# Performance work log

Hardware: AMD Instinct MI355X
Metric: run time of the kernel (lower is better)

## Reference

```python
import jax, jax.numpy as jnp
import numpy as np

B, N_PER, DEG, F_IN, F_HID = 64, 1024, 16, 128, 128
E = B * N_PER * DEG  # 1,048,576 edges, grouped per graph


def setup_inputs() -> dict:
    key = jax.random.key(0)
    ks = jax.random.split(key, 16)
    n_total = B * N_PER
    x = jax.random.normal(ks[0], (n_total, F_IN), dtype=jnp.float32)
    # edges are random within each graph block
    local = jax.random.randint(ks[1], (2, E), 0, N_PER)
    offs = (jnp.arange(E, dtype=jnp.int64) // (N_PER * DEG)) * N_PER
    edge_index = (local.astype(jnp.int64) + offs[None, :])
    edge_weight = jax.random.uniform(ks[2], (E,), dtype=jnp.float32)
    batch_index = jnp.repeat(jnp.arange(B, dtype=jnp.int64), N_PER)
    s = 1.0 / np.sqrt(F_HID)
    params = {
        'W1': jax.random.normal(ks[3], (F_IN, F_HID)) * s,
        'b1': jnp.zeros((F_HID,), jnp.float32),
        'p1': jax.random.normal(ks[4], (F_HID,)) * s,
        'W2': jax.random.normal(ks[5], (F_HID, F_HID)) * s,
        'b2': jnp.zeros((F_HID,), jnp.float32),
        'p2': jax.random.normal(ks[6], (F_HID,)) * s,
        'W3': jax.random.normal(ks[7], (F_HID, F_HID)) * s,
        'b3': jnp.zeros((F_HID,), jnp.float32),
        'p3': jax.random.normal(ks[8], (F_HID,)) * s,
        'Wo': jax.random.normal(ks[9], (2 * F_HID, 1)) * s,
        'bo': jnp.zeros((1,), jnp.float32),
    }
    return {'x': x, 'edge_index': edge_index, 'edge_weight': edge_weight,
            'batch_index': batch_index, **params}


def _gcn_conv(x, src, dst, w, W, b):
    # GCNConv with add_self_loops=True, symmetric normalization, edge_weight.
    n = x.shape[0]
    xW = x @ W
    deg = jnp.zeros((n,), x.dtype).at[dst].add(w) + 1.0  # +1 from self-loop fill
    dinv = jax.lax.rsqrt(deg)
    norm = dinv[src] * w * dinv[dst]
    agg = jnp.zeros_like(xW).at[dst].add(norm[:, None] * xW[src])
    return agg + (dinv * dinv)[:, None] * xW + b  # self-loop term + bias


def _topk_pool(x, src, dst, w, p, n, k):
    # TopKPooling with nonlinearity=sigmoid, equal-size graphs (n -> k nodes).
    f = x.shape[1]
    xr = x.reshape(B, n, f)
    score = jax.nn.sigmoid((xr @ p) / jnp.linalg.norm(p))  # [B, n]
    vals, perm = jax.lax.top_k(score, k)                    # per-graph top-k
    xn = jnp.take_along_axis(xr, perm[:, :, None], axis=1) * vals[:, :, None]
    # inverse map old local idx -> new local idx (-1 if dropped)
    inv = jnp.full((B, n), -1, dtype=jnp.int32)
    inv = inv.at[jnp.arange(B)[:, None], perm].set(jnp.arange(k, dtype=jnp.int32)[None, :])
    g = src // n
    sl = inv[g, src % n]
    dl = inv[dst // n, dst % n]
    keep = (sl >= 0) & (dl >= 0)
    # dropped edges are masked to node 0 with weight 0 (contribute nothing)
    src2 = jnp.where(keep, g * k + sl, 0)
    dst2 = jnp.where(keep, (dst // n) * k + dl, 0)
    w2 = jnp.where(keep, w, jnp.zeros((), w.dtype))
    return xn.reshape(B * k, f), src2, dst2, w2


def reference(x, edge_index, edge_weight, batch_index,
              W1, b1, p1, W2, b2, p2, W3, b3, p3, Wo, bo):
    src, dst = edge_index[0], edge_index[1]
    w = edge_weight
    n = N_PER
    h = _gcn_conv(x, src, dst, w, W1, b1)
    h, src, dst, w = _topk_pool(h, src, dst, w, p1, n, n // 2); n //= 2
    h = jax.nn.relu(h)
    h = _gcn_conv(h, src, dst, w, W2, b2)
    h, src, dst, w = _topk_pool(h, src, dst, w, p2, n, n // 2); n //= 2
    h = jax.nn.relu(h)
    h = _gcn_conv(h, src, dst, w, W3, b3)
    h, src, dst, w = _topk_pool(h, src, dst, w, p3, n, n // 2); n //= 2
    h = jax.nn.relu(h)
    hr = h.reshape(B, n, -1)
    cat = jnp.concatenate([hr.max(axis=1), hr.mean(axis=1)], axis=1)  # gmp || gap
    out = jax.nn.sigmoid(cat @ Wo + bo)
    return out, cat
```

## Files before the change

kernel.cpp:

```cpp
#include <hip/hip_runtime.h>

#define NB 64
#define EDGES 1048576
#define NTOT  65536

struct __align__(8) CsrE { int s; float w; };

using bf16x8 = __attribute__((ext_vector_type(8))) short;
using f32x4  = __attribute__((ext_vector_type(4))) float;

__global__ void k_zerof(float* __restrict__ p, int n){
  int i=blockIdx.x*256+threadIdx.x; if(i<n) p[i]=0.f;
}

__device__ inline void split1(float x, unsigned &hi16, unsigned &lo16){
  unsigned b=__float_as_uint(x);
  unsigned h=(b+0x7FFFu+((b>>16)&1u))&0xFFFF0000u;
  float lf=x-__uint_as_float(h);
  unsigned lb=__float_as_uint(lf);
  hi16=h>>16;
  lo16=(lb+0x7FFFu+((lb>>16)&1u))>>16;
}

__device__ inline void split8(const float4&u, const float4&v, bf16x8&hi, bf16x8&lo){
  float e[8]={u.x,u.y,u.z,u.w,v.x,v.y,v.z,v.w};
  #pragma unroll
  for(int j=0;j<8;++j){
    unsigned h16,l16; split1(e[j],h16,l16);
    hi[j]=(short)h16; lo[j]=(short)l16;
  }
}

__global__ __launch_bounds__(256) void k_wpack(const float* __restrict__ W1,
        const float* __restrict__ W2, const float* __restrict__ W3,
        unsigned* __restrict__ outp){
  int b=blockIdx.x, m=b>>3;
  const float* W = (m==0)?W1:((m==1)?W2:W3);
  unsigned* o = outp + m*16384;
  for(int t=(b&7)*256+threadIdx.x; t<8192; t+=2048){
    int i=t&3, l=(t>>2)&63, c=(t>>8)&7, q=(t>>11)&3;
    int col=c*16+(l&15);
    int k0=q*32+((l>>4)<<3)+i*2;
    float x0=W[k0*128+col], x1=W[(k0+1)*128+col];
    unsigned h0,l0,h1,l1;
    split1(x0,h0,l0); split1(x1,h1,l1);
    int base=((q*8+c)*2)*256;
    o[base + l*4 + i]       = (h1<<16)|h0;
    o[base + 256 + l*4 + i] = (l1<<16)|l0;
  }
}

template<bool G, int S>
__global__ __launch_bounds__(256) void mm_mfma(const float* __restrict__ X,
        const unsigned* __restrict__ Wpk, const int* __restrict__ selold,
        const float* __restrict__ score, float* __restrict__ Y, int gshift){
  __shared__ __align__(16) unsigned Wl[16384];
  const int RPB = 64*S;
  int b=blockIdx.x;
  int row0b;
  if(G){
    int xcd=b&7, slot=b>>3, bpg=1<<gshift;
    int graph=xcd*8+(slot>>gshift), idx=slot&(bpg-1);
    row0b = graph*(bpg*RPB) + idx*RPB;
  } else row0b = b*RPB;
  for(int t=threadIdx.x;t<4096;t+=256)
    ((uint4*)Wl)[t]=((const uint4*)Wpk)[t];
  const int wave=threadIdx.x>>6, lane=threadIdx.x&63;
  const int row0 = row0b + wave*(16*S);
  const int lrow=lane&15, lko=(lane>>4)<<3;
  int orow[S]; float scr[S];
  #pragma unroll
  for(int s=0;s<S;++s){
    int rr=row0+s*16+lrow;
    orow[s]=G?selold[rr]:rr;
    scr[s]=G?score[orow[s]]:1.f;
  }
  const f32x4 vzero={0.f,0.f,0.f,0.f};
  f32x4 acc[S][8];
  #pragma unroll
  for(int s=0;s<S;++s){
    #pragma unroll
    for(int c=0;c<8;++c) acc[s][c]=vzero;
  }
  __syncthreads();
  const char* wb=(const char*)Wl + lane*16;
  float4 u[S],v[S];
  #pragma unroll
  for(int s=0;s<S;++s){
    const float* xp=X+(size_t)orow[s]*128+lko;
    u[s]=*(const float4*)xp; v[s]=*(const float4*)(xp+4);
  }
  #pragma unroll
  for(int q=0;q<4;++q){
    float4 un[S],vn[S];
    if(q<3){
      #pragma unroll
      for(int s=0;s<S;++s){
        const float* xp=X+(size_t)orow[s]*128+(q+1)*32+lko;
        un[s]=*(const float4*)xp; vn[s]=*(const float4*)(xp+4);
      }
    }
    bf16x8 Ah[S],Al[S];
    #pragma unroll
    for(int s=0;s<S;++s){
      if(G){
        u[s].x=fmaxf(u[s].x*scr[s],0.f); u[s].y=fmaxf(u[s].y*scr[s],0.f);
        u[s].z=fmaxf(u[s].z*scr[s],0.f); u[s].w=fmaxf(u[s].w*scr[s],0.f);
        v[s].x=fmaxf(v[s].x*scr[s],0.f); v[s].y=fmaxf(v[s].y*scr[s],0.f);
        v[s].z=fmaxf(v[s].z*scr[s],0.f); v[s].w=fmaxf(v[s].w*scr[s],0.f);
      }
      split8(u[s],v[s],Ah[s],Al[s]);
    }
    #pragma unroll
    for(int c=0;c<8;++c){
      const bf16x8 bh=*(const bf16x8*)(wb + (q*8+c)*2048);
      const bf16x8 bl=*(const bf16x8*)(wb + (q*8+c)*2048 + 1024);
      #pragma unroll
      for(int s=0;s<S;++s){
        acc[s][c]=__builtin_amdgcn_mfma_f32_16x16x32_bf16(Ah[s],bh,acc[s][c],0,0,0);
        acc[s][c]=__builtin_amdgcn_mfma_f32_16x16x32_bf16(Al[s],bh,acc[s][c],0,0,0);
        acc[s][c]=__builtin_amdgcn_mfma_f32_16x16x32_bf16(Ah[s],bl,acc[s][c],0,0,0);
      }
    }
    if(q<3){
      #pragma unroll
      for(int s=0;s<S;++s){ u[s]=un[s]; v[s]=vn[s]; }
    }
  }
  const int dcol=lane&15, dr0=(lane>>4)<<2;
  #pragma unroll
  for(int s=0;s<S;++s){
    #pragma unroll
    for(int c=0;c<8;++c){
      #pragma unroll
      for(int r=0;r<4;++r){
        Y[(size_t)(row0+s*16+dr0+r)*128 + c*16 + dcol]=acc[s][c][r];
      }
    }
  }
}

__global__ __launch_bounds__(1024) void k_count(const int* __restrict__ edst,
        const float* __restrict__ ew, int* __restrict__ chunkcnt, float* __restrict__ chunkw){
  __shared__ int lc[1024];
  __shared__ float lw[1024];
  int b=blockIdx.x, i=threadIdx.x;
  int xcd=b&7, slot=b>>3;
  int graph=xcd*8+(slot&7), chunk=slot>>3;
  int e0=graph*16384+chunk*4096;
  lc[i]=0; lw[i]=0.f;
  __syncthreads();
  for(int e=e0+i; e<e0+4096; e+=1024){
    int dl=edst[e]&1023;
    atomicAdd(&lc[dl],1);
    atomicAdd(&lw[dl],ew[e]);
  }
  __syncthreads();
  chunkcnt[chunk*65536+graph*1024+i]=lc[i];
  chunkw  [chunk*65536+graph*1024+i]=lw[i];
}

__global__ __launch_bounds__(1024) void k_scan_graph(const int* __restrict__ chunkcnt,
        const float* __restrict__ chunkw, int* __restrict__ rowptr,
        float* __restrict__ dinv1, int* __restrict__ chunkfill){
  __shared__ int wsum[16];
  int g=blockIdx.x, i=threadIdx.x;
  int lane=i&63, w=i>>6;
  int o=g*1024+i;
  int c0=chunkcnt[o], c1=chunkcnt[65536+o], c2=chunkcnt[131072+o], c3=chunkcnt[196608+o];
  int c=c0+c1+c2+c3;
  float ws = chunkw[o]+chunkw[65536+o]+chunkw[131072+o]+chunkw[196608+o];
  int v=c;
  #pragma unroll
  for(int off=1;off<64;off<<=1){ int t=__shfl_up(v,off,64); if(lane>=off) v+=t; }
  if(lane==63) wsum[w]=v;
  __syncthreads();
  int base=0;
  for(int k=0;k<w;++k) base+=wsum[k];
  int excl=base+v-c;
  int e0=g*16384;
  int r0=e0+excl;
  rowptr[o]=r0;
  chunkfill[o]       =r0;
  chunkfill[65536+o] =r0+c0;
  chunkfill[131072+o]=r0+c0+c1;
  chunkfill[196608+o]=r0+c0+c1+c2;
  dinv1[o]=rsqrtf(ws+1.0f);
  if(g==63 && i==1023) rowptr[65536]=EDGES;
}

__global__ __launch_bounds__(1024) void k_scatter2(const int* __restrict__ esrc,
        const int* __restrict__ edst, const float* __restrict__ ew,
        const int* __restrict__ chunkfill, CsrE* __restrict__ csr){
  __shared__ int lc[1024];
  int b=blockIdx.x, i=threadIdx.x;
  int xcd=b&7, slot=b>>3;
  int graph=xcd*8+(slot&7), chunk=slot>>3;
  int e0=graph*16384+chunk*4096;
  lc[i]=chunkfill[chunk*65536+graph*1024+i];
  __syncthreads();
  for(int e=e0+i; e<e0+4096; e+=1024){
    int dl=edst[e]&1023;
    int pos=atomicAdd(&lc[dl],1);
    CsrE ce; ce.s=esrc[e]; ce.w=ew[e];
    csr[pos]=ce;
  }
}

template<bool F>
__global__ __launch_bounds__(256) void k_gather(const float* __restrict__ xw, const CsrE* __restrict__ csr,
        const int* __restrict__ rowptr, const int* __restrict__ map, const int* __restrict__ inv,
        const float* __restrict__ dinvv, const float* __restrict__ bias, const float* __restrict__ p,
        float* __restrict__ h, float* __restrict__ score, int gshift, int ns){
  int wv=threadIdx.x>>6, half=(threadIdx.x>>5)&1, hl=threadIdx.x&31;
  int b=blockIdx.x, xcd=b&7, slot=b>>3, bpg=1<<gshift;
  int graph=xcd*8+(slot>>gshift), idx=slot&(bpg-1);
  int v = graph*(bpg<<3) + (idx<<3) + wv*2 + half;
  if(v>=ns) return;
  int d0 = F? map[v] : v;
  float dv=dinvv[v];
  int rs=rowptr[d0], re=rowptr[d0+1];
  const int f4=hl*4;
  float4 accA={0.f,0.f,0.f,0.f}, accB={0.f,0.f,0.f,0.f};
  for(int base=rs; base<re; base+=32){
    int len=re-base; if(len>32) len=32;
    int sidx=0; float cf=0.f;
    if(hl<len){
      CsrE en=csr[base+hl];
      int s=en.s; bool live=true;
      if(F){ int t=inv[s]; live=(t>=0); s=live?t:0; }
      if(live){ sidx=s; cf=dinvv[s]*en.w; }
    }
    int len4=(len+3)&~3;
    for(int j=0;j<len4;j+=4){
      float c0=__shfl(cf,j,32),   c1=__shfl(cf,j+1,32);
      float c2=__shfl(cf,j+2,32), c3=__shfl(cf,j+3,32);
      int   s0=__shfl(sidx,j,32),   s1=__shfl(sidx,j+1,32);
      int   s2=__shfl(sidx,j+2,32), s3=__shfl(sidx,j+3,32);
      const float4 x0=*(const float4*)&xw[(size_t)s0*128+f4];
      const float4 x1=*(const float4*)&xw[(size_t)s1*128+f4];
      const float4 x2=*(const float4*)&xw[(size_t)s2*128+f4];
      const float4 x3=*(const float4*)&xw[(size_t)s3*128+f4];
      accA.x+=c0*x0.x; accA.y+=c0*x0.y; accA.z+=c0*x0.z; accA.w+=c0*x0.w;
      accB.x+=c1*x1.x; accB.y+=c1*x1.y; accB.z+=c1*x1.z; accB.w+=c1*x1.w;
      accA.x+=c2*x2.x; accA.y+=c2*x2.y; accA.z+=c2*x2.z; accA.w+=c2*x2.w;
      accB.x+=c3*x3.x; accB.y+=c3*x3.y; accB.z+=c3*x3.z; accB.w+=c3*x3.w;
    }
  }
  float4 acc; acc.x=accA.x+accB.x; acc.y=accA.y+accB.y;
  acc.z=accA.z+accB.z; acc.w=accA.w+accB.w;
  const float4 xv=*(const float4*)&xw[(size_t)v*128+f4];
  const float4 bv=*(const float4*)&bias[f4];
  float d2=dv*dv;
  float4 hv;
  hv.x=acc.x*dv + d2*xv.x + bv.x;
  hv.y=acc.y*dv + d2*xv.y + bv.y;
  hv.z=acc.z*dv + d2*xv.z + bv.z;
  hv.w=acc.w*dv + d2*xv.w + bv.w;
  *(float4*)&h[(size_t)v*128+f4]=hv;
  const float4 pv=*(const float4*)&p[f4];
  float z=hv.x*pv.x+hv.y*pv.y+hv.z*pv.z+hv.w*pv.w;
  float pp=pv.x*pv.x+pv.y*pv.y+pv.z*pv.z+pv.w*pv.w;
  #pragma unroll
  for(int m=16;m>0;m>>=1){ z+=__shfl_xor(z,m,32); pp+=__shfl_xor(pp,m,32); }
  if(hl==0) score[v]=1.0f/(1.0f+expf(-z/sqrtf(pp)));
}

template<int N, int K, int MODE>
__global__ __launch_bounds__(N) void k_topk(const float* __restrict__ score,
        int* __restrict__ inv, int* __restrict__ selold,
        const int* __restrict__ inv1s, const int* __restrict__ sel1s,
        int* __restrict__ inv12, int* __restrict__ map12,
        const int* __restrict__ rowptr, const CsrE* __restrict__ csr,
        float* __restrict__ dinv_out,
        const float* __restrict__ h3, const float* __restrict__ Wo,
        const float* __restrict__ bo, float* __restrict__ outp){
  __shared__ unsigned hist[256];
  __shared__ int wsum[16];
  __shared__ int c_sh, r_sh;
  __shared__ float red[128];
  int g=blockIdx.x, i=threadIdx.x;
  int lane=i&63, w=i>>6;
  int gv=g*N+i;
  unsigned key=__float_as_uint(score[gv]);
  int st=1;
  int R=K;
  #pragma unroll
  for(int pass=0; pass<4; ++pass){
    int shift=24-pass*8;
    if(i<256) hist[i]=0;
    __syncthreads();
    unsigned byte=(key>>shift)&255u;
    if(st==1) atomicAdd(&hist[byte],1u);
    __syncthreads();
    unsigned hcnt=0, sfx=0;
    if(i<256){
      hcnt=hist[i]; sfx=hcnt;
      #pragma unroll
      for(int off=1;off<64;off<<=1){
        unsigned t=__shfl_down(sfx,off,64);
        if(lane+off<64) sfx+=t;
      }
      if(lane==0) wsum[w]=(int)sfx;
    }
    __syncthreads();
    if(i<256){
      int tot=0;
      for(int k=w+1;k<4;++k) tot+=wsum[k];
      int Si=(int)sfx+tot;
      int A=Si-(int)hcnt;
      if(A<R && R<=Si){ c_sh=i; r_sh=R-A; }
    }
    __syncthreads();
    int c=c_sh; R=r_sh;
    if(st==1){
      if((int)byte>c) st=2;
      else if((int)byte<c) st=0;
    }
    __syncthreads();
  }
  int alive=(st==1)?1:0;
  unsigned long long mA=__ballot(alive);
  int rA=__popcll(mA & ((1ULL<<lane)-1ULL));
  if(lane==0) wsum[w]=__popcll(mA);
  __syncthreads();
  int offA=0;
  for(int k=0;k<w;++k) offA+=wsum[k];
  int tie_rank=offA+rA;
  int sel=(st==2)||(st==1 && tie_rank<R);
  __syncthreads();
  unsigned long long mS=__ballot(sel);
  int rS=__popcll(mS & ((1ULL<<lane)-1ULL));
  if(lane==0) wsum[w]=__popcll(mS);
  __syncthreads();
  int offS=0;
  for(int k=0;k<w;++k) offS+=wsum[k];
  int ng=g*K+offS+rS;
  if(sel && ng<NB*K){ inv[gv]=ng; selold[ng]=gv; }
  else inv[gv]=-1;
  if(MODE==1){
    __syncthreads();
    for(int t=i; t<K; t+=N){
      int v=g*K+t;
      int d0=selold[v];
      int rs=rowptr[d0], re=rowptr[d0+1];
      float s0=0.f,s1=0.f,s2=0.f,s3=0.f;
      int e=rs;
      for(; e+4<=re; e+=4){
        CsrE e0=csr[e], e1=csr[e+1], e2=csr[e+2], e3=csr[e+3];
        if(inv[e0.s]>=0) s0+=e0.w;
        if(inv[e1.s]>=0) s1+=e1.w;
        if(inv[e2.s]>=0) s2+=e2.w;
        if(inv[e3.s]>=0) s3+=e3.w;
      }
      for(; e<re; ++e){
        CsrE en=csr[e];
        if(inv[en.s]>=0) s0+=en.w;
      }
      dinv_out[v]=rsqrtf((s0+s1)+(s2+s3)+1.0f);
    }
  }
  if(MODE==2){
    __syncthreads();
    for(int t=i; t<1024; t+=N){
      int v0=g*1024+t;
      int q=inv1s[v0];
      inv12[v0]=(q>=0)?inv[q]:-1;
    }
    for(int t=i; t<K; t+=N){
      int v=g*K+t;
      map12[v]=sel1s[selold[v]];
    }
    __syncthreads();
    for(int t=i; t<K; t+=N){
      int v=g*K+t;
      int d0=map12[v];
      int rs=rowptr[d0], re=rowptr[d0+1];
      float s0=0.f,s1=0.f,s2=0.f,s3=0.f;
      int e=rs;
      for(; e+4<=re; e+=4){
        CsrE e0=csr[e], e1=csr[e+1], e2=csr[e+2], e3=csr[e+3];
        if(inv12[e0.s]>=0) s0+=e0.w;
        if(inv12[e1.s]>=0) s1+=e1.w;
        if(inv12[e2.s]>=0) s2+=e2.w;
        if(inv12[e3.s]>=0) s3+=e3.w;
      }
      for(; e<re; ++e){
        CsrE en=csr[e];
        if(inv12[en.s]>=0) s0+=en.w;
      }
      dinv_out[v]=rsqrtf((s0+s1)+(s2+s3)+1.0f);
    }
  }
  if(MODE==3){
    __syncthreads();
    int f=i;
    float mx=-3.4e38f, sm=0.f;
    if(f<128){
      for(int nd=0;nd<128;++nd){
        int old=selold[g*128+nd];
        float vv=fmaxf(h3[(size_t)old*128+f]*score[old],0.f);
        mx=fmaxf(mx,vv); sm+=vv;
      }
      float mean=sm*(1.0f/128.0f);
      outp[64+g*256+f]    =mx;
      outp[64+g*256+128+f]=mean;
      red[f]=mx*Wo[f]+mean*Wo[128+f];
    }
    __syncthreads();
    for(int off=64;off>0;off>>=1){
      if(f<off) red[f]+=red[f+off];
      __syncthreads();
    }
    if(f==0){ float z=red[0]+bo[0]; outp[g]=1.0f/(1.0f+expf(-z)); }
  }
}

extern "C" void kernel_launch(void* const* d_in, const int* in_sizes, int n_in,
                              void* d_out, int out_size, void* d_ws, size_t ws_size,
                              hipStream_t stream) {
  (void)in_sizes; (void)n_in;
  const float* x  = (const float*)d_in[0];
  const int*   ei = (const int*)d_in[1];
  const float* ew = (const float*)d_in[2];
  const float* W1=(const float*)d_in[4];  const float* b1=(const float*)d_in[5];  const float* p1=(const float*)d_in[6];
  const float* W2=(const float*)d_in[7];  const float* b2=(const float*)d_in[8];  const float* p2=(const float*)d_in[9];
  const float* W3=(const float*)d_in[10]; const float* b3=(const float*)d_in[11]; const float* p3=(const float*)d_in[12];
  const float* Wo=(const float*)d_in[13]; const float* bo=(const float*)d_in[14];
  float* out=(float*)d_out;

  char* ws=(char*)d_ws;
  size_t cur=0;
  float* slot0=(float*)(ws+cur); cur+=33554432;
  float* slot1=(float*)(ws+cur); cur+=33554432;
  CsrE*  csr  =(CsrE*)(ws+cur);  cur+=(size_t)EDGES*8;
  int*   chunkcnt=(int*)(ws+cur); cur+=1048576;
  float* chunkw  =(float*)(ws+cur); cur+=1048576;
  int*   chunkfill=(int*)(ws+cur); cur+=1048576;
  int*   rowptr=(int*) (ws+cur); cur+=262400;
  float* dinv1=(float*)(ws+cur); cur+=262144;
  float* dinv2=(float*)(ws+cur); cur+=131072;
  float* dinv3=(float*)(ws+cur); cur+=65536;
  float* sc1  =(float*)(ws+cur); cur+=262144;
  float* sc2  =(float*)(ws+cur); cur+=131072;
  float* sc3  =(float*)(ws+cur); cur+=65536;
  int*   inv1 =(int*)  (ws+cur); cur+=262144;
  int*   inv2 =(int*)  (ws+cur); cur+=131072;
  int*   invS =(int*)  (ws+cur); cur+=65536;
  int*   inv12=(int*)  (ws+cur); cur+=262144;
  int*   sel1 =(int*)  (ws+cur); cur+=131072;
  int*   sel2 =(int*)  (ws+cur); cur+=65536;
  int*   sel3 =(int*)  (ws+cur); cur+=32768;
  int*   map12=(int*)  (ws+cur); cur+=65536;
  unsigned* wpk=(unsigned*)(ws+cur); cur+=196608;

  if (ws_size < cur) {
    k_zerof<<<(out_size+255)/256,256,0,stream>>>(out,out_size);
    return;
  }

  const int* esrc=ei; const int* edst=ei+EDGES;

  k_wpack<<<24,256,0,stream>>>(W1,W2,W3,wpk);

  mm_mfma<false,2><<<NTOT/128,256,0,stream>>>(x,wpk,nullptr,nullptr,slot0,0);
  k_count<<<256,1024,0,stream>>>(edst,ew,chunkcnt,chunkw);
  k_scan_graph<<<64,1024,0,stream>>>(chunkcnt,chunkw,rowptr,dinv1,chunkfill);
  k_scatter2<<<256,1024,0,stream>>>(esrc,edst,ew,chunkfill,csr);
  k_gather<false><<<NTOT/8,256,0,stream>>>(slot0,csr,rowptr,nullptr,nullptr,
                                           dinv1,b1,p1,slot1,sc1,7,NTOT);
  k_topk<1024,512,1><<<NB,1024,0,stream>>>(sc1,inv1,sel1,nullptr,nullptr,nullptr,nullptr,
                                           rowptr,csr,dinv2,nullptr,nullptr,nullptr,nullptr);

  mm_mfma<true,1><<<32768/64,256,0,stream>>>(slot1,wpk+16384,sel1,sc1,slot0,3);
  k_gather<true><<<32768/8,256,0,stream>>>(slot0,csr,rowptr,sel1,inv1,
                                           dinv2,b2,p2,slot1,sc2,6,32768);
  k_topk<512,256,2><<<NB,512,0,stream>>>(sc2,inv2,sel2,inv1,sel1,inv12,map12,
                                         rowptr,csr,dinv3,nullptr,nullptr,nullptr,nullptr);

  mm_mfma<true,1><<<16384/64,256,0,stream>>>(slot1,wpk+32768,sel2,sc2,slot0,2);
  k_gather<true><<<16384/8,256,0,stream>>>(slot0,csr,rowptr,map12,inv12,
                                           dinv3,b3,p3,slot1,sc3,5,16384);
  k_topk<256,128,3><<<NB,256,0,stream>>>(sc3,invS,sel3,nullptr,nullptr,nullptr,nullptr,
                                         nullptr,nullptr,nullptr,slot1,Wo,bo,out);
}
```

Baseline: 278.2 us.

## Fuse edge counting with weight packing and merge scan into CSR scatter

```diff
diff --git a/kernel.cpp b/kernel.cpp
--- a/kernel.cpp
+++ b/kernel.cpp
@@ -31,22 +31,44 @@
   }
 }
 
-__global__ __launch_bounds__(256) void k_wpack(const float* __restrict__ W1,
-        const float* __restrict__ W2, const float* __restrict__ W3,
-        unsigned* __restrict__ outp){
-  int b=blockIdx.x, m=b>>3;
-  const float* W = (m==0)?W1:((m==1)?W2:W3);
-  unsigned* o = outp + m*16384;
-  for(int t=(b&7)*256+threadIdx.x; t<8192; t+=2048){
-    int i=t&3, l=(t>>2)&63, c=(t>>8)&7, q=(t>>11)&3;
-    int col=c*16+(l&15);
-    int k0=q*32+((l>>4)<<3)+i*2;
-    float x0=W[k0*128+col], x1=W[(k0+1)*128+col];
-    unsigned h0,l0,h1,l1;
-    split1(x0,h0,l0); split1(x1,h1,l1);
-    int base=((q*8+c)*2)*256;
-    o[base + l*4 + i]       = (h1<<16)|h0;
-    o[base + 256 + l*4 + i] = (l1<<16)|l0;
+__global__ __launch_bounds__(256) void k_cntpack(const int* __restrict__ edst,
+        const float* __restrict__ ew, int* __restrict__ chunkcnt, float* __restrict__ chunkw,
+        const float* __restrict__ W1, const float* __restrict__ W2,
+        const float* __restrict__ W3, unsigned* __restrict__ outp){
+  __shared__ int lc[1024];
+  __shared__ float lw[1024];
+  int b=blockIdx.x, tid=threadIdx.x;
+  if(b<512){
+    int xcd=b&7, slot=b>>3;
+    int graph=xcd*8+(slot&7), chunk=slot>>3;
+    int e0=graph*16384+chunk*2048;
+    for(int t=tid;t<1024;t+=256){ lc[t]=0; lw[t]=0.f; }
+    __syncthreads();
+    for(int e=e0+tid; e<e0+2048; e+=256){
+      int dl=edst[e]&1023;
+      atomicAdd(&lc[dl],1);
+      atomicAdd(&lw[dl],ew[e]);
+    }
+    __syncthreads();
+    for(int t=tid;t<1024;t+=256){
+      chunkcnt[chunk*65536+graph*1024+t]=lc[t];
+      chunkw  [chunk*65536+graph*1024+t]=lw[t];
+    }
+  } else {
+    int wb=b-512, m=wb>>3;
+    const float* W = (m==0)?W1:((m==1)?W2:W3);
+    unsigned* o = outp + m*16384;
+    for(int t=(wb&7)*256+tid; t<8192; t+=2048){
+      int i=t&3, l=(t>>2)&63, c=(t>>8)&7, q=(t>>11)&3;
+      int col=c*16+(l&15);
+      int k0=q*32+((l>>4)<<3)+i*2;
+      float x0=W[k0*128+col], x1=W[(k0+1)*128+col];
+      unsigned h0,l0,h1,l1;
+      split1(x0,h0,l0); split1(x1,h1,l1);
+      int base=((q*8+c)*2)*256;
+      o[base + l*4 + i]       = (h1<<16)|h0;
+      o[base + 256 + l*4 + i] = (l1<<16)|l0;
+    }
   }
 }
 
@@ -140,36 +162,21 @@
   }
 }
 
-__global__ __launch_bounds__(1024) void k_count(const int* __restrict__ edst,
-        const float* __restrict__ ew, int* __restrict__ chunkcnt, float* __restrict__ chunkw){
+__global__ __launch_bounds__(1024) void k_scatter2(const int* __restrict__ esrc,
+        const int* __restrict__ edst, const float* __restrict__ ew,
+        const int* __restrict__ chunkcnt, const float* __restrict__ chunkw,
+        int* __restrict__ rowptr, float* __restrict__ dinv1, CsrE* __restrict__ csr){
   __shared__ int lc[1024];
-  __shared__ float lw[1024];
+  __shared__ int wsum[16];
   int b=blockIdx.x, i=threadIdx.x;
+  int lane=i&63, w=i>>6;
   int xcd=b&7, slot=b>>3;
   int graph=xcd*8+(slot&7), chunk=slot>>3;
-  int e0=graph*16384+chunk*4096;
-  lc[i]=0; lw[i]=0.f;
-  __syncthreads();
-  for(int e=e0+i; e<e0+4096; e+=1024){
-    int dl=edst[e]&1023;
-    atomicAdd(&lc[dl],1);
-    atomicAdd(&lw[dl],ew[e]);
-  }
-  __syncthreads();
-  chunkcnt[chunk*65536+graph*1024+i]=lc[i];
-  chunkw  [chunk*65536+graph*1024+i]=lw[i];
-}
-
-__global__ __launch_bounds__(1024) void k_scan_graph(const int* __restrict__ chunkcnt,
-        const float* __restrict__ chunkw, int* __restrict__ rowptr,
-        float* __restrict__ dinv1, int* __restrict__ chunkfill){
-  __shared__ int wsum[16];
-  int g=blockIdx.x, i=threadIdx.x;
-  int lane=i&63, w=i>>6;
-  int o=g*1024+i;
-  int c0=chunkcnt[o], c1=chunkcnt[65536+o], c2=chunkcnt[131072+o], c3=chunkcnt[196608+o];
-  int c=c0+c1+c2+c3;
-  float ws = chunkw[o]+chunkw[65536+o]+chunkw[131072+o]+chunkw[196608+o];
+  int o=graph*1024+i;
+  int ck[8];
+  int c=0;
+  #pragma unroll
+  for(int k=0;k<8;++k){ ck[k]=chunkcnt[k*65536+o]; c+=ck[k]; }
   int v=c;
   #pragma unroll
   for(int off=1;off<64;off<<=1){ int t=__shfl_up(v,off,64); if(lane>=off) v+=t; }
@@ -178,28 +185,21 @@
   int base=0;
   for(int k=0;k<w;++k) base+=wsum[k];
   int excl=base+v-c;
-  int e0=g*16384;
-  int r0=e0+excl;
-  rowptr[o]=r0;
-  chunkfill[o]       =r0;
-  chunkfill[65536+o] =r0+c0;
-  chunkfill[131072+o]=r0+c0+c1;
-  chunkfill[196608+o]=r0+c0+c1+c2;
-  dinv1[o]=rsqrtf(ws+1.0f);
-  if(g==63 && i==1023) rowptr[65536]=EDGES;
-}
-
-__global__ __launch_bounds__(1024) void k_scatter2(const int* __restrict__ esrc,
-        const int* __restrict__ edst, const float* __restrict__ ew,
-        const int* __restrict__ chunkfill, CsrE* __restrict__ csr){
-  __shared__ int lc[1024];
-  int b=blockIdx.x, i=threadIdx.x;
-  int xcd=b&7, slot=b>>3;
-  int graph=xcd*8+(slot&7), chunk=slot>>3;
-  int e0=graph*16384+chunk*4096;
-  lc[i]=chunkfill[chunk*65536+graph*1024+i];
-  __syncthreads();
-  for(int e=e0+i; e<e0+4096; e+=1024){
+  int r0=graph*16384+excl;
+  if(chunk==0){
+    rowptr[o]=r0;
+    float ws=0.f;
+    #pragma unroll
+    for(int k=0;k<8;++k) ws+=chunkw[k*65536+o];
+    dinv1[o]=rsqrtf(ws+1.0f);
+    if(graph==63 && i==1023) rowptr[65536]=EDGES;
+  }
+  int myfill=r0;
+  for(int k=0;k<chunk;++k) myfill+=ck[k];
+  lc[i]=myfill;
+  __syncthreads();
+  int e0=graph*16384+chunk*2048;
+  for(int e=e0+i; e<e0+2048; e+=1024){
     int dl=edst[e]&1023;
     int pos=atomicAdd(&lc[dl],1);
     CsrE ce; ce.s=esrc[e]; ce.w=ew[e];
@@ -434,9 +434,8 @@
   float* slot0=(float*)(ws+cur); cur+=33554432;
   float* slot1=(float*)(ws+cur); cur+=33554432;
   CsrE*  csr  =(CsrE*)(ws+cur);  cur+=(size_t)EDGES*8;
-  int*   chunkcnt=(int*)(ws+cur); cur+=1048576;
-  float* chunkw  =(float*)(ws+cur); cur+=1048576;
-  int*   chunkfill=(int*)(ws+cur); cur+=1048576;
+  int*   chunkcnt=(int*)(ws+cur); cur+=2097152;
+  float* chunkw  =(float*)(ws+cur); cur+=2097152;
   int*   rowptr=(int*) (ws+cur); cur+=262400;
   float* dinv1=(float*)(ws+cur); cur+=262144;
   float* dinv2=(float*)(ws+cur); cur+=131072;
@@ -461,12 +460,9 @@
 
   const int* esrc=ei; const int* edst=ei+EDGES;
 
-  k_wpack<<<24,256,0,stream>>>(W1,W2,W3,wpk);
-
+  k_cntpack<<<536,256,0,stream>>>(edst,ew,chunkcnt,chunkw,W1,W2,W3,wpk);
   mm_mfma<false,2><<<NTOT/128,256,0,stream>>>(x,wpk,nullptr,nullptr,slot0,0);
-  k_count<<<256,1024,0,stream>>>(edst,ew,chunkcnt,chunkw);
-  k_scan_graph<<<64,1024,0,stream>>>(chunkcnt,chunkw,rowptr,dinv1,chunkfill);
-  k_scatter2<<<256,1024,0,stream>>>(esrc,edst,ew,chunkfill,csr);
+  k_scatter2<<<512,1024,0,stream>>>(esrc,edst,ew,chunkcnt,chunkw,rowptr,dinv1,csr);
   k_gather<false><<<NTOT/8,256,0,stream>>>(slot0,csr,rowptr,nullptr,nullptr,
                                            dinv1,b1,p1,slot1,sc1,7,NTOT);
   k_topk<1024,512,1><<<NB,1024,0,stream>>>(sc1,inv1,sel1,nullptr,nullptr,nullptr,nullptr,
```

After: 270.4 us. 1.03x faster.
